# Kernel optimization log

Measured on AMD Instinct MI355X. Metric: run time of the kernel, lower is better.

## Reference

```python
import jax, jax.numpy as jnp
import numpy as np

D = 1024       # d_model
H = 16         # nhead
DFF = 4096     # dim_feedforward
TM = 512       # T_motion (seq_len)
TA = 512       # T_audio
B = 32         # batch
NBEATS = 64
SIGMA = 4.0    # temporal_sigma
BW = 2.0       # beat_weight
LN_EPS = 1e-5


def setup_inputs() -> dict:
    key = jax.random.key(0)
    ks = jax.random.split(key, 12)
    p = lambda k, shape: jax.random.normal(k, shape, jnp.float32) * 0.02
    return {
        "src": jax.random.normal(ks[0], (TM, B, D), jnp.float32),
        "audio_memory": jax.random.normal(ks[1], (TA, B, D), jnp.float32),
        "beat_frames": jax.random.randint(ks[2], (NBEATS,), 0, TA),
        # self-attention (packed in_proj like nn.MultiheadAttention)
        "sa_in_w": p(ks[3], (3 * D, D)), "sa_in_b": jnp.zeros((3 * D,), jnp.float32),
        "sa_out_w": p(ks[4], (D, D)), "sa_out_b": jnp.zeros((D,), jnp.float32),
        # cross-attention
        "ca_in_w": p(ks[5], (3 * D, D)), "ca_in_b": jnp.zeros((3 * D,), jnp.float32),
        "ca_out_w": p(ks[6], (D, D)), "ca_out_b": jnp.zeros((D,), jnp.float32),
        "gate": jnp.array(0.5, jnp.float32),  # cross_attn_gate (nonzero so branch is active)
        # layernorms
        "n1_g": jnp.ones((D,), jnp.float32), "n1_b": jnp.zeros((D,), jnp.float32),
        "nc_g": jnp.ones((D,), jnp.float32), "nc_b": jnp.zeros((D,), jnp.float32),
        "n2_g": jnp.ones((D,), jnp.float32), "n2_b": jnp.zeros((D,), jnp.float32),
        # FFN
        "lin1_w": p(ks[7], (DFF, D)), "lin1_b": jnp.zeros((DFF,), jnp.float32),
        "lin2_w": p(ks[8], (D, DFF)), "lin2_b": jnp.zeros((D,), jnp.float32),
    }


def _layernorm(x, g, b):
    m = jnp.mean(x, axis=-1, keepdims=True)
    v = jnp.var(x, axis=-1, keepdims=True)
    return (x - m) * jax.lax.rsqrt(v + LN_EPS) * g + b


def _mha(q, k, v, w_in, b_in, w_out, b_out, bias=None):
    # q: (Tq,B,D), k/v: (Tk,B,D); packed in_proj like nn.MultiheadAttention
    hd = D // H
    wq, wk, wv = jnp.split(w_in, 3, axis=0)
    bq, bk, bv = jnp.split(b_in, 3, axis=0)
    def proj(x, w, bb):  # (T,B,D) -> (B,H,T,hd)
        y = jnp.einsum('tbd,ed->tbe', x, w) + bb
        return y.reshape(y.shape[0], y.shape[1], H, hd).transpose(1, 2, 0, 3)
    qh, kh, vh = proj(q, wq, bq), proj(k, wk, bk), proj(v, wv, bv)
    scores = jnp.einsum('bhqd,bhkd->bhqk', qh, kh) / jnp.sqrt(jnp.float32(hd))
    if bias is not None:
        scores = scores + bias[None, None]  # (Tq,Tk) broadcast over (B,H)
    attn = jax.nn.softmax(scores, axis=-1)
    o = jnp.einsum('bhqk,bhkd->bhqd', attn, vh)          # (B,H,Tq,hd)
    o = o.transpose(2, 0, 1, 3).reshape(q.shape[0], q.shape[1], D)  # (Tq,B,D)
    return jnp.einsum('tbd,ed->tbe', o, w_out) + b_out


def _temporal_bias(t_motion, t_audio, sigma):
    scale = (t_audio - 1) / (t_motion - 1) if (t_motion > 1 and t_audio > 1) else 1.0
    audio_pos = jnp.arange(t_motion, dtype=jnp.float32) * scale
    diff = audio_pos[:, None] - jnp.arange(t_audio, dtype=jnp.float32)[None, :]
    return -(diff ** 2) / (2.0 * sigma ** 2)  # (T_motion, T_audio)


def _beat_bias(t_audio, beats, bw):
    # equivalent to sequential torch loop: beat position -> bw, neighbors -> max(., bw/2)
    bias = jnp.zeros((t_audio,), jnp.float32)
    l_idx = jnp.where(beats > 0, beats - 1, 0)
    l_val = jnp.where(beats > 0, bw * 0.5, 0.0)
    r_idx = jnp.where(beats < t_audio - 1, beats + 1, t_audio - 1)
    r_val = jnp.where(beats < t_audio - 1, bw * 0.5, 0.0)
    bias = bias.at[l_idx].max(l_val).at[r_idx].max(r_val).at[beats].max(bw)
    return bias


def reference(src, audio_memory, beat_frames, sa_in_w, sa_in_b, sa_out_w, sa_out_b,
              ca_in_w, ca_in_b, ca_out_w, ca_out_b, gate,
              n1_g, n1_b, nc_g, nc_b, n2_g, n2_b,
              lin1_w, lin1_b, lin2_w, lin2_b):
    # self-attention + residual + LN (dropout is identity in eval)
    x = src + _mha(src, src, src, sa_in_w, sa_in_b, sa_out_w, sa_out_b)
    x = _layernorm(x, n1_g, n1_b)
    # biased cross-attention to audio
    bias = _temporal_bias(TM, TA, SIGMA) + _beat_bias(TA, beat_frames, BW)[None, :]
    cross = _mha(x, audio_memory, audio_memory, ca_in_w, ca_in_b, ca_out_w, ca_out_b, bias)
    x = x + jnp.tanh(gate) * cross
    x = _layernorm(x, nc_g, nc_b)
    # FFN
    h = jax.nn.gelu(jnp.einsum('tbd,fd->tbf', x, lin1_w) + lin1_b, approximate=False)
    ff = jnp.einsum('tbf,df->tbd', h, lin2_w) + lin2_b
    x = _layernorm(x + ff, n2_g, n2_b)
    return x
```

## Files before the change

### kernel.cpp

```cpp
#include <hip/hip_runtime.h>
#include <hip/hip_bf16.h>

#define D_MODEL 1024
#define NHEAD   16
#define HDIM    64
#define DFF_    4096
#define TM_     512
#define TA_     512
#define BATCH   32
#define NTOK    (TM_ * BATCH)
#define NBEATS_ 64

typedef __bf16 bfv8 __attribute__((ext_vector_type(8)));
typedef float  f32x4 __attribute__((ext_vector_type(4)));
typedef unsigned short u16x8 __attribute__((ext_vector_type(8)));
typedef unsigned short u16x4 __attribute__((ext_vector_type(4)));

__device__ __forceinline__ unsigned short f2bf(float f) {
  union { float f; unsigned u; } v; v.f = f;
  unsigned r = v.u + 0x7fffu + ((v.u >> 16) & 1u);
  return (unsigned short)(r >> 16);
}
__device__ __forceinline__ float bf2f(unsigned short h) {
  union { unsigned u; float f; } v; v.u = ((unsigned)h) << 16;
  return v.f;
}
__device__ __forceinline__ unsigned pk2bf(float a, float b) {
  __hip_bfloat162 t = __float22bfloat162_rn(make_float2(a, b));
  union { __hip_bfloat162 h; unsigned u; } v; v.h = t;
  return v.u;
}
__device__ __forceinline__ float gelu_fast(float v) {
  float t = v * v;
  float e = __expf(v * fmaf(0.0713554f, t, 1.5957691f));
  float r = __builtin_amdgcn_rcpf(e + 1.0f);
  return v - v * r;
}

#define GLOAD_LDS16(g, l) __builtin_amdgcn_global_load_lds( \
    (const __attribute__((address_space(1))) unsigned int*)(g), \
    (__attribute__((address_space(3))) unsigned int*)(l), 16, 0, 0)

#define MEMFENCE asm volatile("" ::: "memory")
#define BARRIER  do { MEMFENCE; __builtin_amdgcn_s_barrier(); MEMFENCE; } while (0)

__global__ __launch_bounds__(256) void copy_f32(const float* __restrict__ in, float* __restrict__ out) {
  long i = ((long)blockIdx.x * 256 + threadIdx.x) * 4;
  *(float4*)(out + i) = *(const float4*)(in + i);
}

__global__ __launch_bounds__(256) void cvt_f32_bf16(
    const float* __restrict__ in, unsigned short* __restrict__ out) {
  long i = ((long)blockIdx.x * 256 + threadIdx.x) * 4;
  float4 v = *(const float4*)(in + i);
  u16x4 o = { f2bf(v.x), f2bf(v.y), f2bf(v.z), f2bf(v.w) };
  *(u16x4*)(out + i) = o;
}

__global__ __launch_bounds__(256) void cvt_remap_bt(
    const float* __restrict__ in, unsigned short* __restrict__ out) {
  long rin = blockIdx.x;
  int b = (int)(rin & 31), t = (int)(rin >> 5);
  long rout = (long)b * 512 + t;
  int c = threadIdx.x * 4;
  float4 v = *(const float4*)(in + rin * 1024 + c);
  u16x4 o = { f2bf(v.x), f2bf(v.y), f2bf(v.z), f2bf(v.w) };
  *(u16x4*)(out + rout * 1024 + c) = o;
}

__global__ __launch_bounds__(512) void build_biasT(
    const int* __restrict__ beats, float* __restrict__ biasT) {
  int ta = blockIdx.x;
  int tm = threadIdx.x;
  float m = 0.f;
  for (int i = 0; i < NBEATS_; ++i) {
    int bf = beats[i];
    if (bf == ta) m = fmaxf(m, 2.0f);
    if (bf > 0 && bf - 1 == ta) m = fmaxf(m, 1.0f);
    if (bf < TA_ - 1 && bf + 1 == ta) m = fmaxf(m, 1.0f);
  }
  float diff = (float)tm - (float)ta;
  biasT[ta * TM_ + tm] = -(diff * diff) * (1.0f / 32.0f) + m;
}

template<int EPI, int SWAP>
__global__ __launch_bounds__(512, 2) void gemm256p(
    const unsigned short* __restrict__ A, const unsigned short* __restrict__ Bw,
    const float* __restrict__ bias, int K,
    unsigned short* __restrict__ outP, int ldc,
    unsigned short* __restrict__ dq, unsigned short* __restrict__ dk,
    unsigned short* __restrict__ dv, int s1) {
  __shared__ __align__(16) unsigned short As[2][2][128 * 64];
  __shared__ __align__(16) unsigned short Bs[2][2][128 * 64];
  const int tid = threadIdx.x;
  const int w = tid >> 6, lane = tid & 63;
  const int l15 = lane & 15, l4 = lane >> 4;
  const int wm = w >> 2, wn = w & 3;
  const long m0 = (long)blockIdx.x * 256;
  const long n0 = (long)blockIdx.y * 256;
  const int srow8 = lane >> 3;
  const int scol = ((lane & 7) ^ srow8) * 8;

  auto stageA = [&](int kt, int h) {
    const int k0 = kt * 64, db = kt & 1;
#pragma unroll
    for (int i = 0; i < 2; ++i) {
      int rl = (w * 2 + i) * 8 + srow8;
      GLOAD_LDS16(&A[(m0 + h * 128 + rl) * K + k0 + scol], &As[db][h][(w * 2 + i) * 512]);
    }
  };
  auto stageB = [&](int kt, int h) {
    const int k0 = kt * 64, db = kt & 1;
#pragma unroll
    for (int i = 0; i < 2; ++i) {
      int rl = (w * 2 + i) * 8 + srow8;
      GLOAD_LDS16(&Bw[(n0 + h * 128 + rl) * K + k0 + scol], &Bs[db][h][(w * 2 + i) * 512]);
    }
  };
  auto rdfrag = [&](const unsigned short* buf, int r, int kk) -> bfv8 {
    return *(const bfv8*)&buf[r * 64 + ((((kk << 2) + l4) ^ (l15 & 7)) << 3)];
  };

  f32x4 acc[8][4] = {};
  bfv8 aF[4][2], bF[4][2];
  const int nt = K >> 6;
  const int hB = wn >> 1, rB0 = (wn & 1) * 64;

  stageA(0, 0); stageA(0, 1); stageB(0, 0); stageB(0, 1);
  asm volatile("s_waitcnt vmcnt(0)" ::: "memory");
  BARRIER;

  for (int t = 0; t < nt; ++t) {
    const int db = t & 1;
    const unsigned short* Ah = &As[db][wm][0];
    const unsigned short* Bh = &Bs[db][hB][0];
    const bool pf = (t + 1 < nt);

#pragma unroll
    for (int mf = 0; mf < 4; ++mf) {
      aF[mf][0] = rdfrag(Ah, mf * 16 + l15, 0);
      aF[mf][1] = rdfrag(Ah, mf * 16 + l15, 1);
    }
#pragma unroll
    for (int nf = 0; nf < 2; ++nf) {
      bF[nf][0] = rdfrag(Bh, rB0 + nf * 16 + l15, 0);
      bF[nf][1] = rdfrag(Bh, rB0 + nf * 16 + l15, 1);
    }
    if (pf) { stageA(t + 1, 0); stageA(t + 1, 1); }
    BARRIER;
    asm volatile("s_waitcnt lgkmcnt(0)" ::: "memory");
    __builtin_amdgcn_s_setprio(1);
#pragma unroll
    for (int mf = 0; mf < 4; ++mf)
#pragma unroll
      for (int nf = 0; nf < 2; ++nf)
#pragma unroll
        for (int kk = 0; kk < 2; ++kk)
          acc[mf][nf] = SWAP
            ? __builtin_amdgcn_mfma_f32_16x16x32_bf16(bF[nf][kk], aF[mf][kk], acc[mf][nf], 0, 0, 0)
            : __builtin_amdgcn_mfma_f32_16x16x32_bf16(aF[mf][kk], bF[nf][kk], acc[mf][nf], 0, 0, 0);
    __builtin_amdgcn_s_setprio(0);
    BARRIER;

#pragma unroll
    for (int nf = 2; nf < 4; ++nf) {
      bF[nf][0] = rdfrag(Bh, rB0 + nf * 16 + l15, 0);
      bF[nf][1] = rdfrag(Bh, rB0 + nf * 16 + l15, 1);
    }
    if (pf) { stageB(t + 1, 0); stageB(t + 1, 1); }
    BARRIER;
    asm volatile("s_waitcnt lgkmcnt(0)" ::: "memory");
    __builtin_amdgcn_s_setprio(1);
#pragma unroll
    for (int mf = 0; mf < 4; ++mf)
#pragma unroll
      for (int nf = 2; nf < 4; ++nf)
#pragma unroll
        for (int kk = 0; kk < 2; ++kk)
          acc[mf][nf] = SWAP
            ? __builtin_amdgcn_mfma_f32_16x16x32_bf16(bF[nf][kk], aF[mf][kk], acc[mf][nf], 0, 0, 0)
            : __builtin_amdgcn_mfma_f32_16x16x32_bf16(aF[mf][kk], bF[nf][kk], acc[mf][nf], 0, 0, 0);
    __builtin_amdgcn_s_setprio(0);
    BARRIER;

#pragma unroll
    for (int mf = 0; mf < 4; ++mf) {
      aF[mf][0] = rdfrag(Ah, (mf + 4) * 16 + l15, 0);
      aF[mf][1] = rdfrag(Ah, (mf + 4) * 16 + l15, 1);
    }
    BARRIER;
    asm volatile("s_waitcnt lgkmcnt(0)" ::: "memory");
    __builtin_amdgcn_s_setprio(1);
#pragma unroll
    for (int mf = 0; mf < 4; ++mf)
#pragma unroll
      for (int nf = 0; nf < 2; ++nf)
#pragma unroll
        for (int kk = 0; kk < 2; ++kk)
          acc[mf + 4][nf] = SWAP
            ? __builtin_amdgcn_mfma_f32_16x16x32_bf16(bF[nf][kk], aF[mf][kk], acc[mf + 4][nf], 0, 0, 0)
            : __builtin_amdgcn_mfma_f32_16x16x32_bf16(aF[mf][kk], bF[nf][kk], acc[mf + 4][nf], 0, 0, 0);
    __builtin_amdgcn_s_setprio(0);
    BARRIER;

    __builtin_amdgcn_s_setprio(1);
#pragma unroll
    for (int mf = 0; mf < 4; ++mf)
#pragma unroll
      for (int nf = 2; nf < 4; ++nf)
#pragma unroll
        for (int kk = 0; kk < 2; ++kk)
          acc[mf + 4][nf] = SWAP
            ? __builtin_amdgcn_mfma_f32_16x16x32_bf16(bF[nf][kk], aF[mf][kk], acc[mf + 4][nf], 0, 0, 0)
            : __builtin_amdgcn_mfma_f32_16x16x32_bf16(aF[mf][kk], bF[nf][kk], acc[mf + 4][nf], 0, 0, 0);
    __builtin_amdgcn_s_setprio(0);
    if (pf) asm volatile("s_waitcnt vmcnt(0)" ::: "memory");
    BARRIER;
  }

#pragma unroll
  for (int mf = 0; mf < 8; ++mf)
#pragma unroll
    for (int nf = 0; nf < 4; ++nf) {
      if (SWAP) {
        const int mrow = (int)m0 + wm * 128 + mf * 16 + l15;
        const int col0 = (int)n0 + wn * 64 + nf * 16 + l4 * 4;
        float4 bv = bias ? *(const float4*)&bias[col0] : make_float4(0.f, 0.f, 0.f, 0.f);
        float v0 = acc[mf][nf][0] + bv.x, v1 = acc[mf][nf][1] + bv.y;
        float v2 = acc[mf][nf][2] + bv.z, v3 = acc[mf][nf][3] + bv.w;
        if (EPI == 1) { v0 = gelu_fast(v0); v1 = gelu_fast(v1); v2 = gelu_fast(v2); v3 = gelu_fast(v3); }
        if (EPI == 0 || EPI == 1) {
          uint2 ov; ov.x = pk2bf(v0, v1); ov.y = pk2bf(v2, v3);
          *(uint2*)&outP[(long)mrow * ldc + col0] = ov;
        } else {
          int b_ = mrow >> 9, t_ = mrow & 511;
          if (col0 < s1) {
            int h = col0 >> 6, d0 = col0 & 63;
            uint2 ov; ov.x = pk2bf(v0 * 0.125f, v1 * 0.125f); ov.y = pk2bf(v2 * 0.125f, v3 * 0.125f);
            *(uint2*)&dq[(((long)b_ * NHEAD + h) * TM_ + t_) * HDIM + d0] = ov;
          } else {
            int c0 = col0 - s1, h = c0 >> 6, d0 = c0 & 63;
            uint2 ov; ov.x = pk2bf(v0, v1); ov.y = pk2bf(v2, v3);
            *(uint2*)&dk[(((long)b_ * NHEAD + h) * TA_ + t_) * HDIM + d0] = ov;
          }
        }
      } else {
        const int col = (int)n0 + wn * 64 + nf * 16 + l15;
        const int row0 = (int)m0 + wm * 128 + mf * 16 + l4 * 4;
        float bv = bias ? bias[col] : 0.f;
        int b_ = row0 >> 9, t0 = row0 & 511;
        int h = col >> 6, d = col & 63;
        uint2 ov;
        ov.x = pk2bf(acc[mf][nf][0] + bv, acc[mf][nf][1] + bv);
        ov.y = pk2bf(acc[mf][nf][2] + bv, acc[mf][nf][3] + bv);
        *(uint2*)&dv[(((long)b_ * NHEAD + h) * HDIM + d) * TA_ + t0] = ov;
      }
    }
}

template<int BIAS>
__global__ __launch_bounds__(256) void attn_fused5(
    const unsigned short* __restrict__ Qr, const unsigned short* __restrict__ Kr,
    const unsigned short* __restrict__ Vt, const float* __restrict__ biasT,
    unsigned short* __restrict__ Orow) {
  __shared__ __align__(16) unsigned short Kb[2][64 * 64];
  __shared__ __align__(16) unsigned short Vb[2][64 * 64];
  __shared__ __align__(16) unsigned short P_lds[4][16][64];
  const int flat = blockIdx.y * 8 + blockIdx.x;
  const int W = (flat & 7) * 512 + (flat >> 3);
  const int bh = W >> 3;
  const int b = bh >> 4, h = bh & 15;
  const int tid = threadIdx.x, w = tid >> 6, lane = tid & 63;
  const int l15 = lane & 15, l4 = lane >> 4;
  const int q0 = (W & 7) * 64 + w * 16;

  const unsigned short* Kg = Kr + (long)bh * TA_ * HDIM;
  const unsigned short* Vg = Vt + (long)bh * HDIM * TA_;

  const int stg_row = w * 8 + (lane >> 3);
  const int stg_col = ((lane & 7) ^ (lane >> 3)) * 8;

  auto stage = [&](int t, int cb) {
    const int kv0 = t * 64;
#pragma unroll
    for (int i = 0; i < 2; ++i) {
      int row = i * 32 + stg_row;
      GLOAD_LDS16(Kg + (long)(kv0 + row) * HDIM + stg_col, &Kb[cb][(i * 32 + w * 8) * 64]);
      GLOAD_LDS16(Vg + (long)row * TA_ + kv0 + stg_col,    &Vb[cb][(i * 32 + w * 8) * 64]);
    }
  };

  bfv8 qf[2];
#pragma unroll
  for (int kc = 0; kc < 2; ++kc)
    qf[kc] = *(const bfv8*)&Qr[((long)bh * TM_ + q0 + l15) * HDIM + kc * 32 + l4 * 8];

  float mrun = -1e30f, lrun = 0.f;
  f32x4 o[4] = {};
  unsigned short* prow = &P_lds[w][l15][0];
  const int swz = (l15 & 7) * 8;

  stage(0, 0);
  __syncthreads();
  int cur = 0;

  for (int t = 0; t < 8; ++t) {
    if (t < 7) stage(t + 1, cur ^ 1);
    const int kv0 = t * 64;
    f32x4 s[4] = {};
#pragma unroll
    for (int f = 0; f < 4; ++f) {
#pragma unroll
      for (int kc = 0; kc < 2; ++kc) {
        bfv8 kf = *(const bfv8*)&Kb[cur][(f * 16 + l15) * 64 + (((kc * 4 + l4) * 8) ^ swz)];
        s[f] = __builtin_amdgcn_mfma_f32_16x16x32_bf16(kf, qf[kc], s[f], 0, 0, 0);
      }
    }
    if (BIAS) {
#pragma unroll
      for (int f = 0; f < 4; ++f)
#pragma unroll
        for (int r = 0; r < 4; ++r)
          s[f][r] += biasT[(long)(kv0 + f * 16 + l4 * 4 + r) * TM_ + q0 + l15];
    }
    float tmx = -1e30f;
#pragma unroll
    for (int f = 0; f < 4; ++f)
#pragma unroll
      for (int r = 0; r < 4; ++r) tmx = fmaxf(tmx, s[f][r]);
    tmx = fmaxf(tmx, __shfl_xor(tmx, 16));
    tmx = fmaxf(tmx, __shfl_xor(tmx, 32));
    float newm = fmaxf(mrun, tmx);
    float corr = __expf(mrun - newm);
    lrun *= corr;
#pragma unroll
    for (int fd = 0; fd < 4; ++fd)
#pragma unroll
      for (int r = 0; r < 4; ++r) o[fd][r] *= corr;
    float psum = 0.f;
#pragma unroll
    for (int f = 0; f < 4; ++f) {
#pragma unroll
      for (int r = 0; r < 4; ++r) { float e = __expf(s[f][r] - newm); s[f][r] = e; psum += e; }
      unsigned p0 = pk2bf(s[f][0], s[f][1]);
      unsigned p1 = pk2bf(s[f][2], s[f][3]);
      int blkW = ((f << 1) | (l4 >> 1)) ^ (l15 & 7);
      uint2 pw; pw.x = p0; pw.y = p1;
      *(uint2*)((char*)prow + blkW * 16 + (l4 & 1) * 8) = pw;
    }
    psum += __shfl_xor(psum, 16);
    psum += __shfl_xor(psum, 32);
    lrun += psum;
    mrun = newm;
    asm volatile("s_waitcnt lgkmcnt(0)" ::: "memory");
    __builtin_amdgcn_sched_barrier(0);
#pragma unroll
    for (int c = 0; c < 2; ++c) {
      int blkR = ((c << 2) | l4) ^ (l15 & 7);
      bfv8 pa = *(const bfv8*)((const char*)prow + blkR * 16);
#pragma unroll
      for (int fd = 0; fd < 4; ++fd) {
        bfv8 vb = *(const bfv8*)&Vb[cur][(fd * 16 + l15) * 64 + (((c * 4 + l4) * 8) ^ swz)];
        o[fd] = __builtin_amdgcn_mfma_f32_16x16x32_bf16(vb, pa, o[fd], 0, 0, 0);
      }
    }
    __syncthreads();
    cur ^= 1;
  }

  float invl = 1.f / lrun;
  const long obase = ((long)b * 512 + q0 + l15) * D_MODEL + h * HDIM;
#pragma unroll
  for (int fd = 0; fd < 4; ++fd) {
    uint2 ov;
    ov.x = pk2bf(o[fd][0] * invl, o[fd][1] * invl);
    ov.y = pk2bf(o[fd][2] * invl, o[fd][3] * invl);
    *(uint2*)&Orow[obase + fd * 16 + l4 * 4] = ov;
  }
}

__global__ __launch_bounds__(256) void ln_fused(
    const unsigned short* __restrict__ cin,
    const float* __restrict__ residf, const unsigned short* __restrict__ residb,
    const float* __restrict__ gamma, const float* __restrict__ beta,
    const float* __restrict__ gate,
    float* __restrict__ out_f32, unsigned short* __restrict__ out_bf16,
    int remap_resid, int remap_out) {
  long row = blockIdx.x;
  int t = threadIdx.x;
  int tt = (int)(row & 511), bb = (int)(row >> 9);
  long row_tb = (long)tt * 32 + bb;
  float gf = gate ? tanhf(gate[0]) : 1.0f;
  u16x4 cvb = *(const u16x4*)(cin + row * 1024 + t * 4);
  float c0 = bf2f(cvb[0]), c1 = bf2f(cvb[1]), c2 = bf2f(cvb[2]), c3 = bf2f(cvb[3]);
  float r0, r1, r2, r3;
  if (residf) {
    long rr = remap_resid ? row_tb : row;
    float4 rv = *(const float4*)(residf + rr * 1024 + t * 4);
    r0 = rv.x; r1 = rv.y; r2 = rv.z; r3 = rv.w;
  } else {
    u16x4 rv = *(const u16x4*)(residb + row * 1024 + t * 4);
    r0 = bf2f(rv[0]); r1 = bf2f(rv[1]); r2 = bf2f(rv[2]); r3 = bf2f(rv[3]);
  }
  float y0 = r0 + gf * c0, y1 = r1 + gf * c1, y2 = r2 + gf * c2, y3 = r3 + gf * c3;
  float s = y0 + y1 + y2 + y3;
  float q = y0 * y0 + y1 * y1 + y2 * y2 + y3 * y3;
#pragma unroll
  for (int off = 32; off; off >>= 1) { s += __shfl_xor(s, off); q += __shfl_xor(q, off); }
  __shared__ float sw[4], qw[4];
  int wave = t >> 6;
  if ((t & 63) == 0) { sw[wave] = s; qw[wave] = q; }
  __syncthreads();
  s = sw[0] + sw[1] + sw[2] + sw[3];
  q = qw[0] + qw[1] + qw[2] + qw[3];
  float mean = s * (1.0f / 1024.0f);
  float var = q * (1.0f / 1024.0f) - mean * mean;
  float rstd = rsqrtf(var + 1e-5f);
  float4 g4 = *(const float4*)(gamma + t * 4);
  float4 b4 = *(const float4*)(beta + t * 4);
  float o0 = (y0 - mean) * rstd * g4.x + b4.x;
  float o1 = (y1 - mean) * rstd * g4.y + b4.y;
  float o2 = (y2 - mean) * rstd * g4.z + b4.z;
  float o3 = (y3 - mean) * rstd * g4.w + b4.w;
  if (out_f32) {
    long ro = remap_out ? row_tb : row;
    float4 o = { o0, o1, o2, o3 };
    *(float4*)(out_f32 + ro * 1024 + t * 4) = o;
  }
  if (out_bf16) {
    u16x4 ob = { f2bf(o0), f2bf(o1), f2bf(o2), f2bf(o3) };
    *(u16x4*)(out_bf16 + row * 1024 + t * 4) = ob;
  }
}

static inline char* wsa(char*& p, size_t bytes) {
  char* r = p;
  p += (bytes + 255) & ~(size_t)255;
  return r;
}

extern "C" void kernel_launch(void* const* d_in, const int* in_sizes, int n_in,
                              void* d_out, int out_size, void* d_ws, size_t ws_size,
                              hipStream_t stream) {
  const float* src      = (const float*)d_in[0];
  const float* audio    = (const float*)d_in[1];
  const int*   beats    = (const int*)d_in[2];
  const float* sa_in_w  = (const float*)d_in[3];
  const float* sa_in_b  = (const float*)d_in[4];
  const float* sa_out_w = (const float*)d_in[5];
  const float* sa_out_b = (const float*)d_in[6];
  const float* ca_in_w  = (const float*)d_in[7];
  const float* ca_in_b  = (const float*)d_in[8];
  const float* ca_out_w = (const float*)d_in[9];
  const float* ca_out_b = (const float*)d_in[10];
  const float* gate     = (const float*)d_in[11];
  const float* n1_g     = (const float*)d_in[12];
  const float* n1_b     = (const float*)d_in[13];
  const float* nc_g     = (const float*)d_in[14];
  const float* nc_b     = (const float*)d_in[15];
  const float* n2_g     = (const float*)d_in[16];
  const float* n2_b     = (const float*)d_in[17];
  const float* l1_w     = (const float*)d_in[18];
  const float* l1_b     = (const float*)d_in[19];
  const float* l2_w     = (const float*)d_in[20];
  const float* l2_b     = (const float*)d_in[21];
  float* out = (float*)d_out;
  (void)in_sizes; (void)n_in; (void)out_size;

  const size_t NEEDED = (size_t)236000000;
  if (ws_size < NEEDED) {
    copy_f32<<<dim3(NTOK), dim3(256), 0, stream>>>(src, out);
    return;
  }

  char* p = (char*)d_ws;
  float*          biasT  = (float*)         wsa(p, (size_t)TM_ * TA_ * 4);
  unsigned short* wsaiw  = (unsigned short*)wsa(p, (size_t)3 * D_MODEL * D_MODEL * 2);
  unsigned short* wsaow  = (unsigned short*)wsa(p, (size_t)D_MODEL * D_MODEL * 2);
  unsigned short* wcaiw  = (unsigned short*)wsa(p, (size_t)3 * D_MODEL * D_MODEL * 2);
  unsigned short* wcaow  = (unsigned short*)wsa(p, (size_t)D_MODEL * D_MODEL * 2);
  unsigned short* wl1    = (unsigned short*)wsa(p, (size_t)DFF_ * D_MODEL * 2);
  unsigned short* wl2    = (unsigned short*)wsa(p, (size_t)D_MODEL * DFF_ * 2);
  unsigned short* srcb   = (unsigned short*)wsa(p, (size_t)NTOK * D_MODEL * 2);
  unsigned short* audb   = (unsigned short*)wsa(p, (size_t)NTOK * D_MODEL * 2);
  unsigned short* Qr     = (unsigned short*)wsa(p, (size_t)NTOK * D_MODEL * 2);
  unsigned short* Kr     = (unsigned short*)wsa(p, (size_t)NTOK * D_MODEL * 2);
  unsigned short* Vt     = (unsigned short*)wsa(p, (size_t)NTOK * D_MODEL * 2);
  unsigned short* x1b    = (unsigned short*)wsa(p, (size_t)NTOK * D_MODEL * 2);
  unsigned short* Orow   = srcb;
  unsigned short* C1     = Vt;
  unsigned short* x2b    = audb;
  unsigned short* H1     = Qr;
  unsigned short* C2     = srcb;

  build_biasT<<<dim3(TA_), dim3(TM_), 0, stream>>>(beats, biasT);
  cvt_remap_bt<<<dim3(NTOK), dim3(256), 0, stream>>>(src, srcb);
  cvt_remap_bt<<<dim3(NTOK), dim3(256), 0, stream>>>(audio, audb);
  cvt_f32_bf16<<<dim3((3 * D_MODEL * D_MODEL) / 1024), dim3(256), 0, stream>>>(sa_in_w, wsaiw);
  cvt_f32_bf16<<<dim3((D_MODEL * D_MODEL) / 1024), dim3(256), 0, stream>>>(sa_out_w, wsaow);
  cvt_f32_bf16<<<dim3((3 * D_MODEL * D_MODEL) / 1024), dim3(256), 0, stream>>>(ca_in_w, wcaiw);
  cvt_f32_bf16<<<dim3((D_MODEL * D_MODEL) / 1024), dim3(256), 0, stream>>>(ca_out_w, wcaow);
  cvt_f32_bf16<<<dim3((DFF_ * D_MODEL) / 1024), dim3(256), 0, stream>>>(l1_w, wl1);
  cvt_f32_bf16<<<dim3((D_MODEL * DFF_) / 1024), dim3(256), 0, stream>>>(l2_w, wl2);

  gemm256p<3, 1><<<dim3(64, 8), dim3(512), 0, stream>>>(
      srcb, wsaiw, sa_in_b, 1024, nullptr, 0, Qr, Kr, nullptr, 1024);
  gemm256p<2, 0><<<dim3(64, 4), dim3(512), 0, stream>>>(
      srcb, wsaiw + (size_t)2048 * D_MODEL, sa_in_b + 2048, 1024,
      nullptr, 0, nullptr, nullptr, Vt, 0);
  attn_fused5<0><<<dim3(TM_ / 64, BATCH * NHEAD), dim3(256), 0, stream>>>(Qr, Kr, Vt, nullptr, Orow);
  gemm256p<0, 1><<<dim3(64, 4), dim3(512), 0, stream>>>(
      Orow, wsaow, sa_out_b, 1024, C1, 1024, nullptr, nullptr, nullptr, 0);
  ln_fused<<<dim3(NTOK), dim3(256), 0, stream>>>(
      C1, src, nullptr, n1_g, n1_b, nullptr, nullptr, x1b, 1, 0);

  gemm256p<3, 1><<<dim3(64, 4), dim3(512), 0, stream>>>(
      x1b, wcaiw, ca_in_b, 1024, nullptr, 0, Qr, nullptr, nullptr, 1024);
  gemm256p<3, 1><<<dim3(64, 4), dim3(512), 0, stream>>>(
      audb, wcaiw + (size_t)1024 * D_MODEL, ca_in_b + 1024, 1024,
      nullptr, 0, nullptr, Kr, nullptr, 0);
  gemm256p<2, 0><<<dim3(64, 4), dim3(512), 0, stream>>>(
      audb, wcaiw + (size_t)2048 * D_MODEL, ca_in_b + 2048, 1024,
      nullptr, 0, nullptr, nullptr, Vt, 0);
  attn_fused5<1><<<dim3(TM_ / 64, BATCH * NHEAD), dim3(256), 0, stream>>>(Qr, Kr, Vt, biasT, Orow);
  gemm256p<0, 1><<<dim3(64, 4), dim3(512), 0, stream>>>(
      Orow, wcaow, ca_out_b, 1024, C1, 1024, nullptr, nullptr, nullptr, 0);
  ln_fused<<<dim3(NTOK), dim3(256), 0, stream>>>(
      C1, nullptr, x1b, nc_g, nc_b, gate, nullptr, x2b, 0, 0);

  gemm256p<1, 1><<<dim3(64, 16), dim3(512), 0, stream>>>(
      x2b, wl1, l1_b, 1024, H1, DFF_, nullptr, nullptr, nullptr, 0);
  gemm256p<0, 1><<<dim3(64, 4), dim3(512), 0, stream>>>(
      H1, wl2, l2_b, DFF_, C2, 1024, nullptr, nullptr, nullptr, 0);
  ln_fused<<<dim3(NTOK), dim3(256), 0, stream>>>(
      C2, nullptr, x2b, n2_g, n2_b, nullptr, out, nullptr, 0, 1);
}
```

Before: 1.088 ms.

## Prefetch GEMM tiles two iterations ahead with partial vmcnt waits

Restructures the double-buffered GEMM main loop so global-to-LDS loads for tile t+2 are issued while tile t is computed, and waits only for the older batch of loads (vmcnt(8)) rather than draining all of them. This gives memory latency more time to hide behind MFMA work. The row base pointers and the LDS swizzle offsets are also precomputed to cut address arithmetic in the loop. The B loads for t+2 overwrite the buffer that is currently being read, so correctness depends on the placement of the barriers. With only two LDS buffers this is a risk.

```diff
diff --git a/kernel.cpp b/kernel.cpp
--- a/kernel.cpp
+++ b/kernel.cpp
@@ -101,24 +101,31 @@
   const int srow8 = lane >> 3;
   const int scol = ((lane & 7) ^ srow8) * 8;
 
-  auto stageA = [&](int kt, int h) {
-    const int k0 = kt * 64, db = kt & 1;
-#pragma unroll
-    for (int i = 0; i < 2; ++i) {
-      int rl = (w * 2 + i) * 8 + srow8;
-      GLOAD_LDS16(&A[(m0 + h * 128 + rl) * K + k0 + scol], &As[db][h][(w * 2 + i) * 512]);
-    }
+  const unsigned short* bA00 = A  + (m0 +       (w * 2 + 0) * 8 + srow8) * (long)K + scol;
+  const unsigned short* bA01 = A  + (m0 +       (w * 2 + 1) * 8 + srow8) * (long)K + scol;
+  const unsigned short* bA10 = A  + (m0 + 128 + (w * 2 + 0) * 8 + srow8) * (long)K + scol;
+  const unsigned short* bA11 = A  + (m0 + 128 + (w * 2 + 1) * 8 + srow8) * (long)K + scol;
+  const unsigned short* bB00 = Bw + (n0 +       (w * 2 + 0) * 8 + srow8) * (long)K + scol;
+  const unsigned short* bB01 = Bw + (n0 +       (w * 2 + 1) * 8 + srow8) * (long)K + scol;
+  const unsigned short* bB10 = Bw + (n0 + 128 + (w * 2 + 0) * 8 + srow8) * (long)K + scol;
+  const unsigned short* bB11 = Bw + (n0 + 128 + (w * 2 + 1) * 8 + srow8) * (long)K + scol;
+
+  auto stA = [&](int kt, int h, const unsigned short* p0, const unsigned short* p1) {
+    const int db = kt & 1;
+    const long ko = (long)kt * 64;
+    GLOAD_LDS16(p0 + ko, &As[db][h][(w * 2 + 0) * 512]);
+    GLOAD_LDS16(p1 + ko, &As[db][h][(w * 2 + 1) * 512]);
   };
-  auto stageB = [&](int kt, int h) {
-    const int k0 = kt * 64, db = kt & 1;
-#pragma unroll
-    for (int i = 0; i < 2; ++i) {
-      int rl = (w * 2 + i) * 8 + srow8;
-      GLOAD_LDS16(&Bw[(n0 + h * 128 + rl) * K + k0 + scol], &Bs[db][h][(w * 2 + i) * 512]);
-    }
+  auto stB = [&](int kt, int h, const unsigned short* p0, const unsigned short* p1) {
+    const int db = kt & 1;
+    const long ko = (long)kt * 64;
+    GLOAD_LDS16(p0 + ko, &Bs[db][h][(w * 2 + 0) * 512]);
+    GLOAD_LDS16(p1 + ko, &Bs[db][h][(w * 2 + 1) * 512]);
   };
+  const int swzb0 = ((l4)     ^ (l15 & 7)) << 4;
+  const int swzb1 = ((l4 + 4) ^ (l15 & 7)) << 4;
   auto rdfrag = [&](const unsigned short* buf, int r, int kk) -> bfv8 {
-    return *(const bfv8*)&buf[r * 64 + ((((kk << 2) + l4) ^ (l15 & 7)) << 3)];
+    return *(const bfv8*)((const char*)buf + r * 128 + (kk ? swzb1 : swzb0));
   };
 
   f32x4 acc[8][4] = {};
@@ -126,15 +133,18 @@
   const int nt = K >> 6;
   const int hB = wn >> 1, rB0 = (wn & 1) * 64;
 
-  stageA(0, 0); stageA(0, 1); stageB(0, 0); stageB(0, 1);
-  asm volatile("s_waitcnt vmcnt(0)" ::: "memory");
+  stA(0, 0, bA00, bA01); stA(0, 1, bA10, bA11);
+  stB(0, 0, bB00, bB01); stB(0, 1, bB10, bB11);
+  stB(1, 0, bB00, bB01); stB(1, 1, bB10, bB11);
+  stA(1, 0, bA00, bA01); stA(1, 1, bA10, bA11);
+  asm volatile("s_waitcnt vmcnt(8)" ::: "memory");
   BARRIER;
 
   for (int t = 0; t < nt; ++t) {
     const int db = t & 1;
     const unsigned short* Ah = &As[db][wm][0];
     const unsigned short* Bh = &Bs[db][hB][0];
-    const bool pf = (t + 1 < nt);
+    const bool pf2 = (t + 2 < nt);
 
 #pragma unroll
     for (int mf = 0; mf < 4; ++mf) {
@@ -146,7 +156,6 @@
       bF[nf][0] = rdfrag(Bh, rB0 + nf * 16 + l15, 0);
       bF[nf][1] = rdfrag(Bh, rB0 + nf * 16 + l15, 1);
     }
-    if (pf) { stageA(t + 1, 0); stageA(t + 1, 1); }
     BARRIER;
     asm volatile("s_waitcnt lgkmcnt(0)" ::: "memory");
     __builtin_amdgcn_s_setprio(1);
@@ -167,7 +176,6 @@
       bF[nf][0] = rdfrag(Bh, rB0 + nf * 16 + l15, 0);
       bF[nf][1] = rdfrag(Bh, rB0 + nf * 16 + l15, 1);
     }
-    if (pf) { stageB(t + 1, 0); stageB(t + 1, 1); }
     BARRIER;
     asm volatile("s_waitcnt lgkmcnt(0)" ::: "memory");
     __builtin_amdgcn_s_setprio(1);
@@ -188,6 +196,7 @@
       aF[mf][0] = rdfrag(Ah, (mf + 4) * 16 + l15, 0);
       aF[mf][1] = rdfrag(Ah, (mf + 4) * 16 + l15, 1);
     }
+    if (pf2) { stB(t + 2, 0, bB00, bB01); stB(t + 2, 1, bB10, bB11); }
     BARRIER;
     asm volatile("s_waitcnt lgkmcnt(0)" ::: "memory");
     __builtin_amdgcn_s_setprio(1);
@@ -203,6 +212,7 @@
     __builtin_amdgcn_s_setprio(0);
     BARRIER;
 
+    if (pf2) { stA(t + 2, 0, bA00, bA01); stA(t + 2, 1, bA10, bA11); }
     __builtin_amdgcn_s_setprio(1);
 #pragma unroll
     for (int mf = 0; mf < 4; ++mf)
@@ -214,7 +224,8 @@
             ? __builtin_amdgcn_mfma_f32_16x16x32_bf16(bF[nf][kk], aF[mf][kk], acc[mf + 4][nf], 0, 0, 0)
             : __builtin_amdgcn_mfma_f32_16x16x32_bf16(aF[mf][kk], bF[nf][kk], acc[mf + 4][nf], 0, 0, 0);
     __builtin_amdgcn_s_setprio(0);
-    if (pf) asm volatile("s_waitcnt vmcnt(0)" ::: "memory");
+    if (pf2)                asm volatile("s_waitcnt vmcnt(8)" ::: "memory");
+    else if (t + 1 < nt)    asm volatile("s_waitcnt vmcnt(0)" ::: "memory");
     BARRIER;
   }
 
```

After: 1.049 ms. 3.6% less time.
